# Kernel tuning notes

Hardware: AMD Instinct MI355X
Metric: run time of the kernel (lower is better)

## Reference

```python
import jax, jax.numpy as jnp
import numpy as np

B, L, E, H = 32, 2048, 512, 512


def setup_inputs() -> dict:
    key = jax.random.key(0)
    k1, k2, k3, k4 = jax.random.split(key, 4)
    encodings = jax.random.normal(k1, (B, L, E), dtype=jnp.float32)
    lengths = jax.random.randint(k2, (B,), 1, L + 1, dtype=jnp.int32)
    # Glorot-ish scaled params
    W_h = jax.random.normal(k3, (E, H), dtype=jnp.float32) / np.sqrt(E)
    b_h = jnp.zeros((H,), dtype=jnp.float32)
    W_c = jax.random.normal(k4, (H, E), dtype=jnp.float32) / np.sqrt(H)
    return {"encodings": encodings, "lengths": lengths, "W_h": W_h, "b_h": b_h, "W_c": W_c}


def reference(encodings, lengths, W_h, b_h, W_c):
    # encodings: [B, L, E] padded ragged pack; lengths: [B] valid lengths
    mask = jnp.arange(encodings.shape[1])[None, :] < lengths[:, None]  # [B, L]
    # hidden_layer with tanh nonlinearity (TimeDistributedLinear)
    h = jnp.tanh(jnp.einsum('ble,eh->blh', encodings, W_h) + b_h)  # [B, L, H]
    # context_vector (no bias) -> per-feature attention logits [B, L, E]
    att = jnp.einsum('blh,he->ble', h, W_c)
    # timedistributed_softmax: softmax over time axis per sample, per feature
    att = jnp.where(mask[:, :, None], att, -jnp.inf)
    att = jax.nn.softmax(att, axis=1)  # padded positions get weight 0
    # weighted sum over time -> [B, E], then unsqueeze(1)
    out = jnp.sum(att * encodings, axis=1)[:, None, :]  # [B, 1, E]
    return out
```

## Files before the change

kernel.cpp:

```cpp
#include <hip/hip_runtime.h>
#include <math.h>

#define BB 32
#define LL 2048
#define EE 512
#define HH 512
#define WSL 32

typedef __bf16 bf16_t;
typedef bf16_t bf16x8 __attribute__((ext_vector_type(8)));
typedef float f32x4 __attribute__((ext_vector_type(4)));
typedef unsigned short u16x8 __attribute__((ext_vector_type(8)));

__device__ __forceinline__ unsigned short f2bf(float f) {
  unsigned int u = __builtin_bit_cast(unsigned int, f);
  unsigned int r = (u + 0x7FFFu + ((u >> 16) & 1u)) >> 16;
  return (unsigned short)r;
}
__device__ __forceinline__ float bf2f(unsigned short s) {
  unsigned int u = ((unsigned int)s) << 16;
  return __builtin_bit_cast(float, u);
}
__device__ __forceinline__ bf16x8 ld_frag(const unsigned short* p) {
  u16x8 raw = *(const u16x8*)p;
  return __builtin_bit_cast(bf16x8, raw);
}
__device__ __forceinline__ float tanh_fast(float x) {
  x = fminf(fmaxf(x, -15.f), 15.f);
  float e2 = __expf(2.f * x);
  return (e2 - 1.f) / (e2 + 1.f);
}

__device__ __forceinline__ void w_issue(const unsigned short* __restrict__ Wt,
                                        int rbase, int k0, int lane, u16x8 t[4]) {
  const unsigned short* g = Wt + (size_t)(rbase + (lane >> 2)) * 512 + k0 + (lane & 3) * 8;
#pragma unroll
  for (int i = 0; i < 4; i++) t[i] = *(const u16x8*)(g + i * 16 * 512);
}
__device__ __forceinline__ void w_write(unsigned short* buf, int lane, const u16x8 t[4]) {
  unsigned short* d = buf + (lane >> 2) * WSL + (lane & 3) * 8;
#pragma unroll
  for (int i = 0; i < 4; i++) *(u16x8*)(d + i * 16 * WSL) = t[i];
}

__global__ __launch_bounds__(256) void prep_w(
    const float* __restrict__ Wh, const float* __restrict__ Wc,
    unsigned short* __restrict__ WhT, unsigned short* __restrict__ WcT,
    int* __restrict__ q)
{
  if (blockIdx.x == 0 && blockIdx.y == 0 && threadIdx.x == 0) *q = 0;
  const float* src = blockIdx.y ? Wc : Wh;
  unsigned short* dst = blockIdx.y ? WcT : WhT;
  const int tr = (blockIdx.x >> 3) * 64;
  const int tc = (blockIdx.x & 7) * 64;
  const int tid = threadIdx.x;
  __shared__ float tile[64][65];
  for (int i = tid; i < 64 * 16; i += 256) {
    const int r = i >> 4, c4 = (i & 15) << 2;
    const float4 v = *(const float4*)(src + (size_t)(tr + r) * 512 + tc + c4);
    tile[r][c4 + 0] = v.x; tile[r][c4 + 1] = v.y;
    tile[r][c4 + 2] = v.z; tile[r][c4 + 3] = v.w;
  }
  __syncthreads();
  for (int i = tid; i < 64 * 16; i += 256) {
    const int r = i >> 4, c4 = (i & 15) << 2;
    ushort4 pk;
    pk.x = f2bf(tile[c4 + 0][r]); pk.y = f2bf(tile[c4 + 1][r]);
    pk.z = f2bf(tile[c4 + 2][r]); pk.w = f2bf(tile[c4 + 3][r]);
    *(ushort4*)(dst + (size_t)(tc + r) * 512 + tr + c4) = pk;
  }
}

__global__ __launch_bounds__(512, 2) void attn_main(
    const float* __restrict__ enc, const int* __restrict__ lens,
    const unsigned short* __restrict__ WhT, const float* __restrict__ bh,
    const unsigned short* __restrict__ WcT,
    float* __restrict__ pm, float* __restrict__ ps, float* __restrict__ po,
    int* __restrict__ q, int C, int Lc)
{
  const int tid  = threadIdx.x;
  const int wave = tid >> 6;
  const int lane = tid & 63;
  const int quad = lane >> 4;
  const int l15  = lane & 15;
  const int wbase = wave * 64;

  __shared__ __align__(16) unsigned short encA[32 * 520];
  __shared__ __align__(16) unsigned short hS[32 * 520];
  __shared__ __align__(16) unsigned short wslabS[8 * 2 * 64 * WSL];
  __shared__ __align__(16) float bhS[512];
  __shared__ int itemS;

  unsigned short* buf0 = &wslabS[(wave * 2 + 0) * 64 * WSL];
  unsigned short* buf1 = &wslabS[(wave * 2 + 1) * 64 * WSL];

  bhS[tid] = bh[tid];
  const int nitems = 32 * C;

#pragma unroll 1
  for (;;) {
    __syncthreads();
    if (tid == 0) itemS = atomicAdd(q, 1);
    __syncthreads();
    const int item = itemS;
    if (item >= nitems) break;
    const int b = item & 31;
    const int c = item >> 5;
    const int n = lens[b];
    const int l0 = c * Lc;
    const int nvalid = min(n - l0, Lc);
    if (nvalid <= 0) continue;

    const int phase = (item + wave) & 15;

    float stM[4], stS[4], stO[4];
#pragma unroll
    for (int et = 0; et < 4; et++) { stM[et] = -1e30f; stS[et] = 0.f; stO[et] = 0.f; }

#pragma unroll 1
    for (int r0 = 0; r0 < nvalid; r0 += 32) {
      const float* encRow = enc + ((size_t)b * LL + l0 + r0) * EE;
      for (int i = tid; i < 32 * 128; i += 512) {
        const int m = i >> 7, e4 = (i & 127) << 2;
        const float4 v = *(const float4*)(encRow + (size_t)m * EE + e4);
        ushort4 pk;
        pk.x = f2bf(v.x); pk.y = f2bf(v.y); pk.z = f2bf(v.z); pk.w = f2bf(v.w);
        *(ushort4*)&encA[m * 520 + e4] = pk;
      }
      __syncthreads();

      f32x4 acc1[4][2];
#pragma unroll
      for (int t = 0; t < 4; t++)
        for (int mt = 0; mt < 2; mt++) acc1[t][mt] = (f32x4){0.f, 0.f, 0.f, 0.f};
      {
        u16x8 tA[4], tB[4];
        w_issue(WhT, wbase, ((0 + phase) & 15) * 32, lane, tA);
        w_issue(WhT, wbase, ((1 + phase) & 15) * 32, lane, tB);
        w_write(buf0, lane, tA);
#pragma unroll 1
        for (int kk = 0; kk < 16; kk += 2) {
          w_write(buf1, lane, tB);
          if (kk + 2 < 16) w_issue(WhT, wbase, ((kk + 2 + phase) & 15) * 32, lane, tA);
          {
            const int k0 = ((kk + phase) & 15) * 32;
            const bf16x8 b0 = ld_frag(&encA[l15 * 520 + k0 + quad * 8]);
            const bf16x8 b1 = ld_frag(&encA[(16 + l15) * 520 + k0 + quad * 8]);
#pragma unroll
            for (int t = 0; t < 4; t++) {
              const bf16x8 af = ld_frag(&buf0[(t * 16 + l15) * WSL + quad * 8]);
              acc1[t][0] = __builtin_amdgcn_mfma_f32_16x16x32_bf16(af, b0, acc1[t][0], 0, 0, 0);
              acc1[t][1] = __builtin_amdgcn_mfma_f32_16x16x32_bf16(af, b1, acc1[t][1], 0, 0, 0);
            }
          }
          if (kk + 2 < 16) w_write(buf0, lane, tA);
          if (kk + 3 < 16) w_issue(WhT, wbase, ((kk + 3 + phase) & 15) * 32, lane, tB);
          {
            const int k0 = ((kk + 1 + phase) & 15) * 32;
            const bf16x8 b0 = ld_frag(&encA[l15 * 520 + k0 + quad * 8]);
            const bf16x8 b1 = ld_frag(&encA[(16 + l15) * 520 + k0 + quad * 8]);
#pragma unroll
            for (int t = 0; t < 4; t++) {
              const bf16x8 af = ld_frag(&buf1[(t * 16 + l15) * WSL + quad * 8]);
              acc1[t][0] = __builtin_amdgcn_mfma_f32_16x16x32_bf16(af, b0, acc1[t][0], 0, 0, 0);
              acc1[t][1] = __builtin_amdgcn_mfma_f32_16x16x32_bf16(af, b1, acc1[t][1], 0, 0, 0);
            }
          }
        }
      }

#pragma unroll
      for (int t = 0; t < 4; t++) {
        const f32x4 bv = *(const f32x4*)&bhS[wbase + t * 16 + quad * 4];
#pragma unroll
        for (int mt = 0; mt < 2; mt++) {
          ushort4 pk;
          pk.x = f2bf(tanh_fast(acc1[t][mt][0] + bv[0]));
          pk.y = f2bf(tanh_fast(acc1[t][mt][1] + bv[1]));
          pk.z = f2bf(tanh_fast(acc1[t][mt][2] + bv[2]));
          pk.w = f2bf(tanh_fast(acc1[t][mt][3] + bv[3]));
          *(ushort4*)&hS[(mt * 16 + l15) * 520 + wbase + t * 16 + quad * 4] = pk;
        }
      }
      __syncthreads();

      f32x4 acc2[2][4];
#pragma unroll
      for (int mt = 0; mt < 2; mt++)
        for (int et = 0; et < 4; et++) acc2[mt][et] = (f32x4){0.f, 0.f, 0.f, 0.f};
      {
        u16x8 tA[4], tB[4];
        w_issue(WcT, wbase, ((0 + phase) & 15) * 32, lane, tA);
        w_issue(WcT, wbase, ((1 + phase) & 15) * 32, lane, tB);
        w_write(buf0, lane, tA);
#pragma unroll 1
        for (int kk = 0; kk < 16; kk += 2) {
          w_write(buf1, lane, tB);
          if (kk + 2 < 16) w_issue(WcT, wbase, ((kk + 2 + phase) & 15) * 32, lane, tA);
          {
            const int k0 = ((kk + phase) & 15) * 32;
            const bf16x8 a0 = ld_frag(&hS[l15 * 520 + k0 + quad * 8]);
            const bf16x8 a1 = ld_frag(&hS[(16 + l15) * 520 + k0 + quad * 8]);
#pragma unroll
            for (int et = 0; et < 4; et++) {
              const bf16x8 bf = ld_frag(&buf0[(et * 16 + l15) * WSL + quad * 8]);
              acc2[0][et] = __builtin_amdgcn_mfma_f32_16x16x32_bf16(a0, bf, acc2[0][et], 0, 0, 0);
              acc2[1][et] = __builtin_amdgcn_mfma_f32_16x16x32_bf16(a1, bf, acc2[1][et], 0, 0, 0);
            }
          }
          if (kk + 2 < 16) w_write(buf0, lane, tA);
          if (kk + 3 < 16) w_issue(WcT, wbase, ((kk + 3 + phase) & 15) * 32, lane, tB);
          {
            const int k0 = ((kk + 1 + phase) & 15) * 32;
            const bf16x8 a0 = ld_frag(&hS[l15 * 520 + k0 + quad * 8]);
            const bf16x8 a1 = ld_frag(&hS[(16 + l15) * 520 + k0 + quad * 8]);
#pragma unroll
            for (int et = 0; et < 4; et++) {
              const bf16x8 bf = ld_frag(&buf1[(et * 16 + l15) * WSL + quad * 8]);
              acc2[0][et] = __builtin_amdgcn_mfma_f32_16x16x32_bf16(a0, bf, acc2[0][et], 0, 0, 0);
              acc2[1][et] = __builtin_amdgcn_mfma_f32_16x16x32_bf16(a1, bf, acc2[1][et], 0, 0, 0);
            }
          }
        }
      }

      bool ok[2][4];
#pragma unroll
      for (int mt = 0; mt < 2; mt++)
#pragma unroll
        for (int r = 0; r < 4; r++)
          ok[mt][r] = (r0 + mt * 16 + quad * 4 + r) < nvalid;

#pragma unroll
      for (int et = 0; et < 4; et++) {
        const int e = wbase + et * 16 + l15;
        float v[2][4];
        float lm = -1e30f;
#pragma unroll
        for (int mt = 0; mt < 2; mt++)
#pragma unroll
          for (int r = 0; r < 4; r++) {
            v[mt][r] = ok[mt][r] ? acc2[mt][et][r] : -1e30f;
            lm = fmaxf(lm, v[mt][r]);
          }
        lm = fmaxf(lm, __shfl_xor(lm, 16));
        lm = fmaxf(lm, __shfl_xor(lm, 32));
        float ls = 0.f, lo = 0.f;
#pragma unroll
        for (int mt = 0; mt < 2; mt++)
#pragma unroll
          for (int r = 0; r < 4; r++) {
            const float p  = __expf(v[mt][r] - lm);
            const float ev = bf2f(encA[(mt * 16 + quad * 4 + r) * 520 + e]);
            ls += p;
            lo += p * ev;
          }
        ls += __shfl_xor(ls, 16); ls += __shfl_xor(ls, 32);
        lo += __shfl_xor(lo, 16); lo += __shfl_xor(lo, 32);
        const float Mn = fmaxf(stM[et], lm);
        const float sc = __expf(stM[et] - Mn);
        const float st = __expf(lm - Mn);
        stS[et] = stS[et] * sc + ls * st;
        stO[et] = stO[et] * sc + lo * st;
        stM[et] = Mn;
      }
      __syncthreads();
    }

    if (quad == 0) {
      const size_t base = ((size_t)b * C + c) * EE;
#pragma unroll
      for (int et = 0; et < 4; et++) {
        const int e = wbase + et * 16 + l15;
        pm[base + e] = stM[et];
        ps[base + e] = stS[et];
        po[base + e] = stO[et];
      }
    }
  }
}

__global__ __launch_bounds__(256) void attn_combine(
    const float* __restrict__ pm, const float* __restrict__ ps,
    const float* __restrict__ po, const int* __restrict__ lens,
    float* __restrict__ out, int C, int Lc)
{
  const int b  = blockIdx.y;
  const int e  = blockIdx.x * 64 + (threadIdx.x & 63);
  const int g  = threadIdx.x >> 6;
  const int n  = lens[b];
  const int cmax = min(C, (n + Lc - 1) / Lc);

  float M = -1e30f, S = 0.f, O = 0.f;
  for (int c = g; c < cmax; c += 4) {
    const size_t base = ((size_t)b * C + c) * EE;
    const float m = pm[base + e];
    const float s = ps[base + e];
    const float o = po[base + e];
    const float Mn  = fmaxf(M, m);
    const float sc0 = __expf(M - Mn);
    const float sc1 = __expf(m - Mn);
    S = S * sc0 + s * sc1;
    O = O * sc0 + o * sc1;
    M = Mn;
  }

  __shared__ float sM[4][64], sS[4][64], sO[4][64];
  sM[g][threadIdx.x & 63] = M;
  sS[g][threadIdx.x & 63] = S;
  sO[g][threadIdx.x & 63] = O;
  __syncthreads();

  if (g == 0) {
    const int le = threadIdx.x & 63;
    float Mt = sM[0][le], St = sS[0][le], Ot = sO[0][le];
#pragma unroll
    for (int gg = 1; gg < 4; gg++) {
      const float m = sM[gg][le];
      const float Mn  = fmaxf(Mt, m);
      const float sc0 = __expf(Mt - Mn);
      const float sc1 = __expf(m - Mn);
      St = St * sc0 + sS[gg][le] * sc1;
      Ot = Ot * sc0 + sO[gg][le] * sc1;
      Mt = Mn;
    }
    out[(size_t)b * EE + e] = Ot / St;
  }
}

extern "C" void kernel_launch(void* const* d_in, const int* in_sizes, int n_in,
                              void* d_out, int out_size, void* d_ws, size_t ws_size,
                              hipStream_t stream) {
  const float* enc  = (const float*)d_in[0];
  const int*   lens = (const int*)d_in[1];
  const float* Wh   = (const float*)d_in[2];
  const float* bh   = (const float*)d_in[3];
  const float* Wc   = (const float*)d_in[4];
  float* out = (float*)d_out;

  const size_t wbytes = (size_t)512 * 512 * sizeof(unsigned short);
  int C = 64;
  while (C > 8 && ws_size < (size_t)3 * BB * C * EE * sizeof(float) + 2 * wbytes + 64)
    C >>= 1;
  const int Lc = LL / C;

  float* pm = (float*)d_ws;
  float* ps = pm + (size_t)BB * C * EE;
  float* po = ps + (size_t)BB * C * EE;
  unsigned short* WhT = (unsigned short*)(po + (size_t)BB * C * EE);
  unsigned short* WcT = WhT + (size_t)512 * 512;
  int* q = (int*)(WcT + (size_t)512 * 512);

  prep_w<<<dim3(64, 2), 256, 0, stream>>>(Wh, Wc, WhT, WcT, q);
  attn_main<<<dim3(512), 512, 0, stream>>>(enc, lens, WhT, bh, WcT, pm, ps, po, q, C, Lc);
  attn_combine<<<dim3(8, BB), 256, 0, stream>>>(pm, ps, po, lens, out, C, Lc);
}
```

Before: 292.8 us.

## Load weight MFMA fragments directly from global memory, drop LDS weight staging

Weight fragments for both GEMMs are now loaded straight from global (L2-resident) memory into registers in MFMA operand layout, replacing the per-wave LDS double buffer. This removes the LDS write/read round trip for the weights and frees 64KB of shared memory. Launch bounds now request 4 blocks per SM instead of 2 to use the freed LDS for occupancy. The risks are more register pressure under the tighter occupancy target and less coalesced 16-byte global loads per lane.

```diff
diff --git a/kernel.cpp b/kernel.cpp
--- a/kernel.cpp
+++ b/kernel.cpp
@@ -5,7 +5,6 @@
 #define LL 2048
 #define EE 512
 #define HH 512
-#define WSL 32
 
 typedef __bf16 bf16_t;
 typedef bf16_t bf16x8 __attribute__((ext_vector_type(8)));
@@ -31,16 +30,10 @@
   return (e2 - 1.f) / (e2 + 1.f);
 }
 
-__device__ __forceinline__ void w_issue(const unsigned short* __restrict__ Wt,
-                                        int rbase, int k0, int lane, u16x8 t[4]) {
-  const unsigned short* g = Wt + (size_t)(rbase + (lane >> 2)) * 512 + k0 + (lane & 3) * 8;
-#pragma unroll
-  for (int i = 0; i < 4; i++) t[i] = *(const u16x8*)(g + i * 16 * 512);
-}
-__device__ __forceinline__ void w_write(unsigned short* buf, int lane, const u16x8 t[4]) {
-  unsigned short* d = buf + (lane >> 2) * WSL + (lane & 3) * 8;
-#pragma unroll
-  for (int i = 0; i < 4; i++) *(u16x8*)(d + i * 16 * WSL) = t[i];
+__device__ __forceinline__ void frag_issue(const unsigned short* __restrict__ g,
+                                           int k0, bf16x8 f[4]) {
+#pragma unroll
+  for (int i = 0; i < 4; i++) f[i] = ld_frag(g + (size_t)i * 16 * 512 + k0);
 }
 
 __global__ __launch_bounds__(256) void prep_w(
@@ -71,7 +64,7 @@
   }
 }
 
-__global__ __launch_bounds__(512, 2) void attn_main(
+__global__ __launch_bounds__(512, 4) void attn_main(
     const float* __restrict__ enc, const int* __restrict__ lens,
     const unsigned short* __restrict__ WhT, const float* __restrict__ bh,
     const unsigned short* __restrict__ WcT,
@@ -87,12 +80,8 @@
 
   __shared__ __align__(16) unsigned short encA[32 * 520];
   __shared__ __align__(16) unsigned short hS[32 * 520];
-  __shared__ __align__(16) unsigned short wslabS[8 * 2 * 64 * WSL];
   __shared__ __align__(16) float bhS[512];
   __shared__ int itemS;
-
-  unsigned short* buf0 = &wslabS[(wave * 2 + 0) * 64 * WSL];
-  unsigned short* buf1 = &wslabS[(wave * 2 + 1) * 64 * WSL];
 
   bhS[tid] = bh[tid];
   const int nitems = 32 * C;
@@ -134,37 +123,33 @@
       for (int t = 0; t < 4; t++)
         for (int mt = 0; mt < 2; mt++) acc1[t][mt] = (f32x4){0.f, 0.f, 0.f, 0.f};
       {
-        u16x8 tA[4], tB[4];
-        w_issue(WhT, wbase, ((0 + phase) & 15) * 32, lane, tA);
-        w_issue(WhT, wbase, ((1 + phase) & 15) * 32, lane, tB);
-        w_write(buf0, lane, tA);
+        const unsigned short* baseW = WhT + (size_t)(wbase + l15) * 512 + quad * 8;
+        bf16x8 fA[4], fB[4];
+        frag_issue(baseW, ((0 + phase) & 15) * 32, fA);
+        frag_issue(baseW, ((1 + phase) & 15) * 32, fB);
 #pragma unroll 1
         for (int kk = 0; kk < 16; kk += 2) {
-          w_write(buf1, lane, tB);
-          if (kk + 2 < 16) w_issue(WhT, wbase, ((kk + 2 + phase) & 15) * 32, lane, tA);
           {
             const int k0 = ((kk + phase) & 15) * 32;
             const bf16x8 b0 = ld_frag(&encA[l15 * 520 + k0 + quad * 8]);
             const bf16x8 b1 = ld_frag(&encA[(16 + l15) * 520 + k0 + quad * 8]);
 #pragma unroll
             for (int t = 0; t < 4; t++) {
-              const bf16x8 af = ld_frag(&buf0[(t * 16 + l15) * WSL + quad * 8]);
-              acc1[t][0] = __builtin_amdgcn_mfma_f32_16x16x32_bf16(af, b0, acc1[t][0], 0, 0, 0);
-              acc1[t][1] = __builtin_amdgcn_mfma_f32_16x16x32_bf16(af, b1, acc1[t][1], 0, 0, 0);
+              acc1[t][0] = __builtin_amdgcn_mfma_f32_16x16x32_bf16(fA[t], b0, acc1[t][0], 0, 0, 0);
+              acc1[t][1] = __builtin_amdgcn_mfma_f32_16x16x32_bf16(fA[t], b1, acc1[t][1], 0, 0, 0);
             }
-          }
-          if (kk + 2 < 16) w_write(buf0, lane, tA);
-          if (kk + 3 < 16) w_issue(WhT, wbase, ((kk + 3 + phase) & 15) * 32, lane, tB);
+            if (kk + 2 < 16) frag_issue(baseW, ((kk + 2 + phase) & 15) * 32, fA);
+          }
           {
             const int k0 = ((kk + 1 + phase) & 15) * 32;
             const bf16x8 b0 = ld_frag(&encA[l15 * 520 + k0 + quad * 8]);
             const bf16x8 b1 = ld_frag(&encA[(16 + l15) * 520 + k0 + quad * 8]);
 #pragma unroll
             for (int t = 0; t < 4; t++) {
-              const bf16x8 af = ld_frag(&buf1[(t * 16 + l15) * WSL + quad * 8]);
-              acc1[t][0] = __builtin_amdgcn_mfma_f32_16x16x32_bf16(af, b0, acc1[t][0], 0, 0, 0);
-              acc1[t][1] = __builtin_amdgcn_mfma_f32_16x16x32_bf16(af, b1, acc1[t][1], 0, 0, 0);
+              acc1[t][0] = __builtin_amdgcn_mfma_f32_16x16x32_bf16(fB[t], b0, acc1[t][0], 0, 0, 0);
+              acc1[t][1] = __builtin_amdgcn_mfma_f32_16x16x32_bf16(fB[t], b1, acc1[t][1], 0, 0, 0);
             }
+            if (kk + 3 < 16) frag_issue(baseW, ((kk + 3 + phase) & 15) * 32, fB);
           }
         }
       }
@@ -189,37 +174,33 @@
       for (int mt = 0; mt < 2; mt++)
         for (int et = 0; et < 4; et++) acc2[mt][et] = (f32x4){0.f, 0.f, 0.f, 0.f};
       {
-        u16x8 tA[4], tB[4];
-        w_issue(WcT, wbase, ((0 + phase) & 15) * 32, lane, tA);
-        w_issue(WcT, wbase, ((1 + phase) & 15) * 32, lane, tB);
-        w_write(buf0, lane, tA);
+        const unsigned short* baseW = WcT + (size_t)(wbase + l15) * 512 + quad * 8;
+        bf16x8 fA[4], fB[4];
+        frag_issue(baseW, ((0 + phase) & 15) * 32, fA);
+        frag_issue(baseW, ((1 + phase) & 15) * 32, fB);
 #pragma unroll 1
         for (int kk = 0; kk < 16; kk += 2) {
-          w_write(buf1, lane, tB);
-          if (kk + 2 < 16) w_issue(WcT, wbase, ((kk + 2 + phase) & 15) * 32, lane, tA);
           {
             const int k0 = ((kk + phase) & 15) * 32;
             const bf16x8 a0 = ld_frag(&hS[l15 * 520 + k0 + quad * 8]);
             const bf16x8 a1 = ld_frag(&hS[(16 + l15) * 520 + k0 + quad * 8]);
 #pragma unroll
             for (int et = 0; et < 4; et++) {
-              const bf16x8 bf = ld_frag(&buf0[(et * 16 + l15) * WSL + quad * 8]);
-              acc2[0][et] = __builtin_amdgcn_mfma_f32_16x16x32_bf16(a0, bf, acc2[0][et], 0, 0, 0);
-              acc2[1][et] = __builtin_amdgcn_mfma_f32_16x16x32_bf16(a1, bf, acc2[1][et], 0, 0, 0);
+              acc2[0][et] = __builtin_amdgcn_mfma_f32_16x16x32_bf16(a0, fA[et], acc2[0][et], 0, 0, 0);
+              acc2[1][et] = __builtin_amdgcn_mfma_f32_16x16x32_bf16(a1, fA[et], acc2[1][et], 0, 0, 0);
             }
-          }
-          if (kk + 2 < 16) w_write(buf0, lane, tA);
-          if (kk + 3 < 16) w_issue(WcT, wbase, ((kk + 3 + phase) & 15) * 32, lane, tB);
+            if (kk + 2 < 16) frag_issue(baseW, ((kk + 2 + phase) & 15) * 32, fA);
+          }
           {
             const int k0 = ((kk + 1 + phase) & 15) * 32;
             const bf16x8 a0 = ld_frag(&hS[l15 * 520 + k0 + quad * 8]);
             const bf16x8 a1 = ld_frag(&hS[(16 + l15) * 520 + k0 + quad * 8]);
 #pragma unroll
             for (int et = 0; et < 4; et++) {
-              const bf16x8 bf = ld_frag(&buf1[(et * 16 + l15) * WSL + quad * 8]);
-              acc2[0][et] = __builtin_amdgcn_mfma_f32_16x16x32_bf16(a0, bf, acc2[0][et], 0, 0, 0);
-              acc2[1][et] = __builtin_amdgcn_mfma_f32_16x16x32_bf16(a1, bf, acc2[1][et], 0, 0, 0);
+              acc2[0][et] = __builtin_amdgcn_mfma_f32_16x16x32_bf16(a0, fB[et], acc2[0][et], 0, 0, 0);
+              acc2[1][et] = __builtin_amdgcn_mfma_f32_16x16x32_bf16(a1, fB[et], acc2[1][et], 0, 0, 0);
             }
+            if (kk + 3 < 16) frag_issue(baseW, ((kk + 3 + phase) & 15) * 32, fB);
           }
         }
       }
```

After: 369.7 us. +26.2%, slower.

## Prefetch next work item's first encoding tile into registers across items

Applied to the files above, without the earlier changes.

The persistent kernel now claims its next work item early, on the last pass of the current item, and skips items that have no valid rows while claiming. After the second GEMM it loads the next item's first 32-row encoding tile into registers, so that global load overlaps the softmax epilogue and the partial-result stores. The encA and hS shared buffers are merged into one ping-pong pair so the prefetched tile can be written into the slot hS freed. The grid is halved to 256 blocks, and the 32 extra registers for the prefetch may lower occupancy or limit latency hiding.

```diff
diff --git a/kernel.cpp b/kernel.cpp
--- a/kernel.cpp
+++ b/kernel.cpp
@@ -85,47 +85,86 @@
   const int l15  = lane & 15;
   const int wbase = wave * 64;
 
-  __shared__ __align__(16) unsigned short encA[32 * 520];
-  __shared__ __align__(16) unsigned short hS[32 * 520];
+  __shared__ __align__(16) unsigned short ebuf[2][32 * 520];
   __shared__ __align__(16) unsigned short wslabS[8 * 2 * 64 * WSL];
   __shared__ __align__(16) float bhS[512];
   __shared__ int itemS;
 
-  unsigned short* buf0 = &wslabS[(wave * 2 + 0) * 64 * WSL];
-  unsigned short* buf1 = &wslabS[(wave * 2 + 1) * 64 * WSL];
+  unsigned short* sl0 = &wslabS[(wave * 2 + 0) * 64 * WSL];
+  unsigned short* sl1 = &wslabS[(wave * 2 + 1) * 64 * WSL];
 
   bhS[tid] = bh[tid];
   const int nitems = 32 * C;
 
+  if (tid == 0) {
+    int it;
+    for (;;) {
+      it = atomicAdd(q, 1);
+      if (it >= nitems || lens[it & 31] > (it >> 5) * Lc) break;
+    }
+    itemS = it;
+  }
+  __syncthreads();
+  int item = itemS;
+  int p = 0;
+
+  float4 eR[8];
+  if (item < nitems) {
+    const float* src = enc + ((size_t)(item & 31) * LL + (size_t)(item >> 5) * Lc) * EE;
+#pragma unroll
+    for (int k = 0; k < 8; k++) {
+      const int i = tid + k * 512;
+      eR[k] = *(const float4*)(src + (size_t)(i >> 7) * EE + ((i & 127) << 2));
+    }
+  }
+
 #pragma unroll 1
   for (;;) {
-    __syncthreads();
-    if (tid == 0) itemS = atomicAdd(q, 1);
-    __syncthreads();
-    const int item = itemS;
     if (item >= nitems) break;
     const int b = item & 31;
     const int c = item >> 5;
-    const int n = lens[b];
     const int l0 = c * Lc;
-    const int nvalid = min(n - l0, Lc);
-    if (nvalid <= 0) continue;
-
+    const int nvalid = min(lens[b] - l0, Lc);
     const int phase = (item + wave) & 15;
+    unsigned short* encA = ebuf[p];
+    unsigned short* hS   = ebuf[p ^ 1];
 
     float stM[4], stS[4], stO[4];
 #pragma unroll
     for (int et = 0; et < 4; et++) { stM[et] = -1e30f; stS[et] = 0.f; stO[et] = 0.f; }
+
+    int nextItem = nitems;
 
 #pragma unroll 1
     for (int r0 = 0; r0 < nvalid; r0 += 32) {
-      const float* encRow = enc + ((size_t)b * LL + l0 + r0) * EE;
-      for (int i = tid; i < 32 * 128; i += 512) {
-        const int m = i >> 7, e4 = (i & 127) << 2;
-        const float4 v = *(const float4*)(encRow + (size_t)m * EE + e4);
-        ushort4 pk;
-        pk.x = f2bf(v.x); pk.y = f2bf(v.y); pk.z = f2bf(v.z); pk.w = f2bf(v.w);
-        *(ushort4*)&encA[m * 520 + e4] = pk;
+      const bool lastPass = (r0 + 32 >= nvalid);
+
+      if (r0 == 0) {
+#pragma unroll
+        for (int k = 0; k < 8; k++) {
+          const int i = tid + k * 512;
+          const float4 v = eR[k];
+          ushort4 pk;
+          pk.x = f2bf(v.x); pk.y = f2bf(v.y); pk.z = f2bf(v.z); pk.w = f2bf(v.w);
+          *(ushort4*)&encA[(i >> 7) * 520 + ((i & 127) << 2)] = pk;
+        }
+      } else {
+        const float* encRow = enc + ((size_t)b * LL + l0 + r0) * EE;
+        for (int i = tid; i < 32 * 128; i += 512) {
+          const int m = i >> 7, e4 = (i & 127) << 2;
+          const float4 v = *(const float4*)(encRow + (size_t)m * EE + e4);
+          ushort4 pk;
+          pk.x = f2bf(v.x); pk.y = f2bf(v.y); pk.z = f2bf(v.z); pk.w = f2bf(v.w);
+          *(ushort4*)&encA[m * 520 + e4] = pk;
+        }
+      }
+      if (lastPass && tid == 0) {
+        int it;
+        for (;;) {
+          it = atomicAdd(q, 1);
+          if (it >= nitems || lens[it & 31] > (it >> 5) * Lc) break;
+        }
+        itemS = it;
       }
       __syncthreads();
 
@@ -137,10 +176,10 @@
         u16x8 tA[4], tB[4];
         w_issue(WhT, wbase, ((0 + phase) & 15) * 32, lane, tA);
         w_issue(WhT, wbase, ((1 + phase) & 15) * 32, lane, tB);
-        w_write(buf0, lane, tA);
+        w_write(sl0, lane, tA);
 #pragma unroll 1
         for (int kk = 0; kk < 16; kk += 2) {
-          w_write(buf1, lane, tB);
+          w_write(sl1, lane, tB);
           if (kk + 2 < 16) w_issue(WhT, wbase, ((kk + 2 + phase) & 15) * 32, lane, tA);
           {
             const int k0 = ((kk + phase) & 15) * 32;
@@ -148,12 +187,12 @@
             const bf16x8 b1 = ld_frag(&encA[(16 + l15) * 520 + k0 + quad * 8]);
 #pragma unroll
             for (int t = 0; t < 4; t++) {
-              const bf16x8 af = ld_frag(&buf0[(t * 16 + l15) * WSL + quad * 8]);
+              const bf16x8 af = ld_frag(&sl0[(t * 16 + l15) * WSL + quad * 8]);
               acc1[t][0] = __builtin_amdgcn_mfma_f32_16x16x32_bf16(af, b0, acc1[t][0], 0, 0, 0);
               acc1[t][1] = __builtin_amdgcn_mfma_f32_16x16x32_bf16(af, b1, acc1[t][1], 0, 0, 0);
             }
           }
-          if (kk + 2 < 16) w_write(buf0, lane, tA);
+          if (kk + 2 < 16) w_write(sl0, lane, tA);
           if (kk + 3 < 16) w_issue(WhT, wbase, ((kk + 3 + phase) & 15) * 32, lane, tB);
           {
             const int k0 = ((kk + 1 + phase) & 15) * 32;
@@ -161,7 +200,7 @@
             const bf16x8 b1 = ld_frag(&encA[(16 + l15) * 520 + k0 + quad * 8]);
 #pragma unroll
             for (int t = 0; t < 4; t++) {
-              const bf16x8 af = ld_frag(&buf1[(t * 16 + l15) * WSL + quad * 8]);
+              const bf16x8 af = ld_frag(&sl1[(t * 16 + l15) * WSL + quad * 8]);
               acc1[t][0] = __builtin_amdgcn_mfma_f32_16x16x32_bf16(af, b0, acc1[t][0], 0, 0, 0);
               acc1[t][1] = __builtin_amdgcn_mfma_f32_16x16x32_bf16(af, b1, acc1[t][1], 0, 0, 0);
             }
@@ -192,10 +231,10 @@
         u16x8 tA[4], tB[4];
         w_issue(WcT, wbase, ((0 + phase) & 15) * 32, lane, tA);
         w_issue(WcT, wbase, ((1 + phase) & 15) * 32, lane, tB);
-        w_write(buf0, lane, tA);
+        w_write(sl0, lane, tA);
 #pragma unroll 1
         for (int kk = 0; kk < 16; kk += 2) {
-          w_write(buf1, lane, tB);
+          w_write(sl1, lane, tB);
           if (kk + 2 < 16) w_issue(WcT, wbase, ((kk + 2 + phase) & 15) * 32, lane, tA);
           {
             const int k0 = ((kk + phase) & 15) * 32;
@@ -203,12 +242,12 @@
             const bf16x8 a1 = ld_frag(&hS[(16 + l15) * 520 + k0 + quad * 8]);
 #pragma unroll
             for (int et = 0; et < 4; et++) {
-              const bf16x8 bf = ld_frag(&buf0[(et * 16 + l15) * WSL + quad * 8]);
+              const bf16x8 bf = ld_frag(&sl0[(et * 16 + l15) * WSL + quad * 8]);
               acc2[0][et] = __builtin_amdgcn_mfma_f32_16x16x32_bf16(a0, bf, acc2[0][et], 0, 0, 0);
               acc2[1][et] = __builtin_amdgcn_mfma_f32_16x16x32_bf16(a1, bf, acc2[1][et], 0, 0, 0);
             }
           }
-          if (kk + 2 < 16) w_write(buf0, lane, tA);
+          if (kk + 2 < 16) w_write(sl0, lane, tA);
           if (kk + 3 < 16) w_issue(WcT, wbase, ((kk + 3 + phase) & 15) * 32, lane, tB);
           {
             const int k0 = ((kk + 1 + phase) & 15) * 32;
@@ -216,10 +255,22 @@
             const bf16x8 a1 = ld_frag(&hS[(16 + l15) * 520 + k0 + quad * 8]);
 #pragma unroll
             for (int et = 0; et < 4; et++) {
-              const bf16x8 bf = ld_frag(&buf1[(et * 16 + l15) * WSL + quad * 8]);
+              const bf16x8 bf = ld_frag(&sl1[(et * 16 + l15) * WSL + quad * 8]);
               acc2[0][et] = __builtin_amdgcn_mfma_f32_16x16x32_bf16(a0, bf, acc2[0][et], 0, 0, 0);
               acc2[1][et] = __builtin_amdgcn_mfma_f32_16x16x32_bf16(a1, bf, acc2[1][et], 0, 0, 0);
             }
+          }
+        }
+      }
+
+      if (lastPass) {
+        nextItem = itemS;
+        if (nextItem < nitems) {
+          const float* src = enc + ((size_t)(nextItem & 31) * LL + (size_t)(nextItem >> 5) * Lc) * EE;
+#pragma unroll
+          for (int k = 0; k < 8; k++) {
+            const int i = tid + k * 512;
+            eR[k] = *(const float4*)(src + (size_t)(i >> 7) * EE + ((i & 127) << 2));
           }
         }
       }
@@ -250,10 +301,10 @@
         for (int mt = 0; mt < 2; mt++)
 #pragma unroll
           for (int r = 0; r < 4; r++) {
-            const float p  = __expf(v[mt][r] - lm);
+            const float pexp = __expf(v[mt][r] - lm);
             const float ev = bf2f(encA[(mt * 16 + quad * 4 + r) * 520 + e]);
-            ls += p;
-            lo += p * ev;
+            ls += pexp;
+            lo += pexp * ev;
           }
         ls += __shfl_xor(ls, 16); ls += __shfl_xor(ls, 32);
         lo += __shfl_xor(lo, 16); lo += __shfl_xor(lo, 32);
@@ -277,6 +328,9 @@
         po[base + e] = stO[et];
       }
     }
+
+    item = nextItem;
+    p ^= 1;
   }
 }
 
@@ -352,6 +406,6 @@
   int* q = (int*)(WcT + (size_t)512 * 512);
 
   prep_w<<<dim3(64, 2), 256, 0, stream>>>(Wh, Wc, WhT, WcT, q);
-  attn_main<<<dim3(512), 512, 0, stream>>>(enc, lens, WhT, bh, WcT, pm, ps, po, q, C, Lc);
+  attn_main<<<dim3(256), 512, 0, stream>>>(enc, lens, WhT, bh, WcT, pm, ps, po, q, C, Lc);
   attn_combine<<<dim3(8, BB), 256, 0, stream>>>(pm, ps, po, lens, out, C, Lc);
 }
```

Measured after the change: 276.7 us. 1.06x faster.
